# Kernel tuning notes

Measured on AMD Instinct MI355X. Metric: run time of the kernel, lower is better.

The kernel has to match this reference:

```python
import jax, jax.numpy as jnp
import numpy as np

MODEL_DIM = 1024
NUM_HEADS = 16
D_K = MODEL_DIM // NUM_HEADS  # 64
MAX_SEQ_LEN = 3200
B, T = 2, 2048
THETA_BASE = 10000.0


def setup_inputs() -> dict:
    key = jax.random.key(0)
    ks = jax.random.split(key, 5)
    scale = 1.0 / np.sqrt(MODEL_DIM)
    x = jax.random.normal(ks[0], (B, T, MODEL_DIM), dtype=jnp.float32)
    wq = jax.random.normal(ks[1], (MODEL_DIM, MODEL_DIM), dtype=jnp.float32) * scale
    wk = jax.random.normal(ks[2], (MODEL_DIM, MODEL_DIM), dtype=jnp.float32) * scale
    wv = jax.random.normal(ks[3], (MODEL_DIM, MODEL_DIM), dtype=jnp.float32) * scale
    wo = jax.random.normal(ks[4], (MODEL_DIM, MODEL_DIM), dtype=jnp.float32) * scale
    bq = jnp.zeros((MODEL_DIM,), jnp.float32)
    bk = jnp.zeros((MODEL_DIM,), jnp.float32)
    bv = jnp.zeros((MODEL_DIM,), jnp.float32)
    bo = jnp.zeros((MODEL_DIM,), jnp.float32)
    # RoPE tables, exactly as precompute_rotation_matrix: theta duplicated
    # adjacently ([t0,t0,t1,t1,...]).
    theta = THETA_BASE ** (jnp.arange(D_K // 2, dtype=jnp.float32) * (-2.0 / D_K))
    ang = jnp.outer(jnp.arange(MAX_SEQ_LEN, dtype=jnp.float32), theta)  # [L, d/2]
    ang = jnp.repeat(ang, 2, axis=-1)  # [L, d]
    return {
        "x": x, "wq": wq, "bq": bq, "wk": wk, "bk": bk,
        "wv": wv, "bv": bv, "wo": wo, "bo": bo,
        "cos": jnp.cos(ang), "sin": jnp.sin(ang),
    }


def reference(x, wq, bq, wk, bk, wv, bv, wo, bo, cos, sin):
    b, t, dm = x.shape
    h, d = NUM_HEADS, dm // NUM_HEADS

    # NOTE: original uses .view(b, h, t, d) directly on [b, t, h*d] (no
    # transpose) — a nonstandard head split we replicate faithfully.
    xq = (x @ wq.T + bq).reshape(b, h, t, d)
    xk = (x @ wk.T + bk).reshape(b, h, t, d)
    xv = (x @ wv.T + bv).reshape(b, h, t, d)

    def rot_half(q):
        # pairs are adjacent (2i, 2i+1): out[2i] = -q[2i+1], out[2i+1] = q[2i]
        q2 = q.reshape(b, h, t, d // 2, 2)
        return jnp.stack([-q2[..., 1], q2[..., 0]], axis=-1).reshape(b, h, t, d)

    # NOTE: original indexes cos/sin at the single position `seq_len`
    # (rotation_matrix_cos[:, :, xq.shape[2], :]), broadcasting one row over
    # all positions — replicated faithfully.
    c = cos[t]  # [d]
    s = sin[t]  # [d]
    xq = xq * c + rot_half(xq) * s
    xk = xk * c + rot_half(xk) * s

    scores = jnp.einsum("bhqd,bhkd->bhqk", xq, xk) / np.sqrt(d)
    p = jax.nn.softmax(scores, axis=-1)  # mask='none', dropout=0.0
    o = jnp.einsum("bhqk,bhkd->bhqd", p, xv)
    o = o.transpose(0, 2, 1, 3).reshape(b, t, dm)  # 'b h t d -> b t (h d)'
    return o @ wo.T + bo
```

## Files before the change

### kernel.cpp

```cpp
#include <hip/hip_runtime.h>

typedef _Float16 half8 __attribute__((ext_vector_type(8)));
typedef __fp16 pkh2 __attribute__((ext_vector_type(2)));
typedef float floatx4 __attribute__((ext_vector_type(4)));

#define AS1 __attribute__((address_space(1)))
#define AS3 __attribute__((address_space(3)))


__global__ __launch_bounds__(256) void convert_kernel(
    const float* __restrict__ x, const float* __restrict__ wq,
    const float* __restrict__ wk, const float* __restrict__ wv,
    const float* __restrict__ wo,
    _Float16* __restrict__ xb, _Float16* __restrict__ wqkv,
    _Float16* __restrict__ wob)
{
    int i = (blockIdx.x * 256 + threadIdx.x) * 4;
    const float* src; _Float16* dst; int off;
    if (i < 4194304)      { src = x;  dst = xb;            off = i; }
    else if (i < 5242880) { src = wq; dst = wqkv;          off = i - 4194304; }
    else if (i < 6291456) { src = wk; dst = wqkv + 1048576; off = i - 5242880; }
    else if (i < 7340032) { src = wv; dst = wqkv + 2097152; off = i - 6291456; }
    else                  { src = wo; dst = wob;           off = i - 7340032; }
    float4 v = *(const float4*)(src + off);
    union { uint2 u; pkh2 h[2]; } o;
    o.h[0] = __builtin_amdgcn_cvt_pkrtz(v.x, v.y);
    o.h[1] = __builtin_amdgcn_cvt_pkrtz(v.z, v.w);
    *(uint2*)(dst + off) = o.u;
}

template<bool QKV>
__global__ __launch_bounds__(256) void gemm_kernel(
    const _Float16* __restrict__ A, const _Float16* __restrict__ W,
    const float* __restrict__ b0, const float* __restrict__ b1,
    const float* __restrict__ b2,
    const float* __restrict__ cosr, const float* __restrict__ sinr,
    _Float16* __restrict__ O0, _Float16* __restrict__ O1,
    _Float16* __restrict__ O2, float* __restrict__ Of)
{
    __shared__ __align__(16) _Float16 As[128 * 64];
    __shared__ __align__(16) _Float16 Bs[128 * 64];
    const int tid  = threadIdx.x;
    const int lane = tid & 63, w = tid >> 6;
    const int lrow = lane & 15, quad = lane >> 4;
    const int wr = (w & 1) * 64, wc = (w >> 1) * 64;
    const int arow0 = blockIdx.x * 128;
    const int brow0 = blockIdx.y * 128;

    const int r8 = lane >> 3;
    const int gcol = ((lane & 7) ^ r8) * 8;

    floatx4 acc[4][4] = {};

    for (int kk = 0; kk < 1024; kk += 64) {
        __syncthreads();
        for (int u = 0; u < 4; u++) {
            const int row = w * 32 + u * 8;
            __builtin_amdgcn_global_load_lds(
                (const AS1 unsigned*)(const void*)(A + (size_t)(arow0 + row + r8) * 1024 + kk + gcol),
                (AS3 unsigned*)(void*)(As + row * 64), 16, 0, 0);
            __builtin_amdgcn_global_load_lds(
                (const AS1 unsigned*)(const void*)(W + (size_t)(brow0 + row + r8) * 1024 + kk + gcol),
                (AS3 unsigned*)(void*)(Bs + row * 64), 16, 0, 0);
        }
        __syncthreads();
        for (int ks = 0; ks < 2; ks++) {
            const int swz = ((ks * 4 + quad) ^ (lrow & 7)) * 8;
            half8 af[4], bf[4];
            for (int mt = 0; mt < 4; mt++)
                af[mt] = *(const half8*)&As[(wr + mt * 16 + lrow) * 64 + swz];
            for (int nt = 0; nt < 4; nt++)
                bf[nt] = *(const half8*)&Bs[(wc + nt * 16 + lrow) * 64 + swz];
            for (int mt = 0; mt < 4; mt++)
                for (int nt = 0; nt < 4; nt++)
                    acc[mt][nt] = __builtin_amdgcn_mfma_f32_16x16x32_f16(
                        af[mt], bf[nt], acc[mt][nt], 0, 0, 0);
        }
    }

    if (QKV) {
        const int seg = blockIdx.y >> 3;
        const float* bias = seg == 0 ? b0 : (seg == 1 ? b1 : b2);
        _Float16* out = seg == 0 ? O0 : (seg == 1 ? O1 : O2);
        const int nbase = (blockIdx.y & 7) * 128 + wc;
        for (int nt = 0; nt < 4; nt++) {
            const int n = nbase + nt * 16 + lrow;
            const float bv = bias[n];
            const int dj = n & 63;
            const float cv = cosr[dj], sv = sinr[dj];
            const bool odd = (n & 1) != 0;
            for (int mt = 0; mt < 4; mt++)
                for (int r = 0; r < 4; r++) {
                    float v = acc[mt][nt][r] + bv;
                    if (seg < 2) {
                        float p = __shfl_xor(v, 1, 64);
                        v = odd ? (v * cv + p * sv) : (v * cv - p * sv);
                    }
                    if (seg == 0) v *= 0.125f;
                    int row = arow0 + wr + mt * 16 + quad * 4 + r;
                    out[row * 1024 + n] = (_Float16)v;
                }
        }
    } else {
        const int nbase = blockIdx.y * 128 + wc;
        for (int nt = 0; nt < 4; nt++) {
            const int n = nbase + nt * 16 + lrow;
            const float bv = b0[n];
            for (int mt = 0; mt < 4; mt++)
                for (int r = 0; r < 4; r++) {
                    int row = arow0 + wr + mt * 16 + quad * 4 + r;
                    Of[row * 1024 + n] = acc[mt][nt][r] + bv;
                }
        }
    }
}

__global__ __launch_bounds__(256) void vtrans_kernel(
    const _Float16* __restrict__ V, _Float16* __restrict__ VT)
{
    __shared__ __align__(16) _Float16 T[64][72];
    const int tid = threadIdx.x;
    const int kt = blockIdx.x;
    const int bh = blockIdx.y;
    const int bi = bh >> 4, hi = bh & 15;
    const _Float16* Vh = V + (size_t)(bi * 2048 + hi * 128) * 1024 + kt * 4096;
    const int srow = tid >> 3, sblk = tid & 7;
    union { uint4 u; _Float16 h[8]; } a, b;
    a.u = *(const uint4*)(Vh + (2 * srow) * 64 + sblk * 8);
    b.u = *(const uint4*)(Vh + (2 * srow + 1) * 64 + sblk * 8);
    for (int j = 0; j < 8; j++) {
        union { unsigned u; _Float16 h[2]; } pk;
        pk.h[0] = a.h[j]; pk.h[1] = b.h[j];
        *(unsigned*)&T[sblk * 8 + j][2 * srow] = pk.u;
    }
    __syncthreads();
    const int d = tid >> 2, c = tid & 3;
    _Float16* out = VT + ((size_t)bh * 64 + d) * 2048 + kt * 64 + c * 16;
    *(uint4*)(out)     = *(const uint4*)&T[d][c * 16];
    *(uint4*)(out + 8) = *(const uint4*)&T[d][c * 16 + 8];
}

__global__ __launch_bounds__(256, 3) void attn_kernel(
    const _Float16* __restrict__ Q, const _Float16* __restrict__ K,
    const _Float16* __restrict__ VT, _Float16* __restrict__ O)
{
    __shared__ __align__(16) _Float16 Ks[2][64][72];
    __shared__ __align__(16) _Float16 Vts[2][64][72];
    __shared__ __align__(16) _Float16 Pt[4][32][40];

    const int tid  = threadIdx.x;
    const int lane = tid & 63, w = tid >> 6;
    const int lrow = lane & 15, quad = lane >> 4;
    const int qt = blockIdx.x, bh = blockIdx.y;
    const int bi = bh >> 4, hi = bh & 15;
    const size_t base = (size_t)(bi * 2048 + hi * 128) * 1024;
    const _Float16* Qh  = Q + base;
    const _Float16* Kh  = K + base;
    const _Float16* VTh = VT + (size_t)bh * 131072;

    half8 qf[2][2];
    for (int nt = 0; nt < 2; nt++)
        for (int ks = 0; ks < 2; ks++)
            qf[nt][ks] = *(const half8*)(Qh + (qt * 128 + w * 32 + nt * 16 + lrow) * 64
                                          + ks * 32 + quad * 8);

    floatx4 oacc[4][2] = {};
    float lsum0 = 0.0f, lsum1 = 0.0f;

    const int srow = tid >> 3, sblk = tid & 7;
    const int vd = tid >> 2, vc = tid & 3;

    {
        *(uint4*)&Ks[0][srow][sblk * 8]      = *(const uint4*)(Kh + srow * 64 + sblk * 8);
        *(uint4*)&Ks[0][srow + 32][sblk * 8] = *(const uint4*)(Kh + (srow + 32) * 64 + sblk * 8);
        const _Float16* vsrc = VTh + (size_t)vd * 2048 + vc * 16;
        *(uint4*)&Vts[0][vd][vc * 16]     = *(const uint4*)(vsrc);
        *(uint4*)&Vts[0][vd][vc * 16 + 8] = *(const uint4*)(vsrc + 8);
    }
    __syncthreads();

    const float LOG2E = 1.44269504f;
    const float OFF   = -8.65617025f;

    for (int kt = 0; kt < 32; kt++) {
        const int cur = kt & 1;
        uint4 k0, k1, v0, v1;
        if (kt < 31) {
            const _Float16* Kt = Kh + (kt + 1) * 4096;
            const _Float16* Vt = VTh + (size_t)vd * 2048 + (kt + 1) * 64 + vc * 16;
            k0 = *(const uint4*)(Kt + srow * 64 + sblk * 8);
            k1 = *(const uint4*)(Kt + (srow + 32) * 64 + sblk * 8);
            v0 = *(const uint4*)(Vt);
            v1 = *(const uint4*)(Vt + 8);
        }
        for (int h = 0; h < 2; h++) {
            for (int k2 = 0; k2 < 2; k2++) {
                const int kt4 = h * 2 + k2;
                floatx4 s0 = {}, s1 = {};
                for (int ks = 0; ks < 2; ks++) {
                    half8 af = *(const half8*)&Ks[cur][kt4 * 16 + lrow][ks * 32 + quad * 8];
                    s0 = __builtin_amdgcn_mfma_f32_16x16x32_f16(af, qf[0][ks], s0, 0, 0, 0);
                    s1 = __builtin_amdgcn_mfma_f32_16x16x32_f16(af, qf[1][ks], s1, 0, 0, 0);
                }
                float p00 = __builtin_amdgcn_exp2f(fmaf(s0[0], LOG2E, OFF));
                float p01 = __builtin_amdgcn_exp2f(fmaf(s0[1], LOG2E, OFF));
                float p02 = __builtin_amdgcn_exp2f(fmaf(s0[2], LOG2E, OFF));
                float p03 = __builtin_amdgcn_exp2f(fmaf(s0[3], LOG2E, OFF));
                float p10 = __builtin_amdgcn_exp2f(fmaf(s1[0], LOG2E, OFF));
                float p11 = __builtin_amdgcn_exp2f(fmaf(s1[1], LOG2E, OFF));
                float p12 = __builtin_amdgcn_exp2f(fmaf(s1[2], LOG2E, OFF));
                float p13 = __builtin_amdgcn_exp2f(fmaf(s1[3], LOG2E, OFF));
                lsum0 += p00 + p01 + p02 + p03;
                lsum1 += p10 + p11 + p12 + p13;
                union { uint2 u; pkh2 h2[2]; } pk0, pk1;
                pk0.h2[0] = __builtin_amdgcn_cvt_pkrtz(p00, p01);
                pk0.h2[1] = __builtin_amdgcn_cvt_pkrtz(p02, p03);
                pk1.h2[0] = __builtin_amdgcn_cvt_pkrtz(p10, p11);
                pk1.h2[1] = __builtin_amdgcn_cvt_pkrtz(p12, p13);
                *(uint2*)&Pt[w][lrow][k2 * 16 + quad * 4]      = pk0.u;
                *(uint2*)&Pt[w][16 + lrow][k2 * 16 + quad * 4] = pk1.u;
            }
            half8 bf0 = *(const half8*)&Pt[w][lrow][quad * 8];
            half8 bf1 = *(const half8*)&Pt[w][16 + lrow][quad * 8];
            for (int dt = 0; dt < 4; dt++) {
                half8 av = *(const half8*)&Vts[cur][dt * 16 + lrow][h * 32 + quad * 8];
                oacc[dt][0] = __builtin_amdgcn_mfma_f32_16x16x32_f16(av, bf0, oacc[dt][0], 0, 0, 0);
                oacc[dt][1] = __builtin_amdgcn_mfma_f32_16x16x32_f16(av, bf1, oacc[dt][1], 0, 0, 0);
            }
        }
        if (kt < 31) {
            const int nxt = cur ^ 1;
            *(uint4*)&Ks[nxt][srow][sblk * 8]      = k0;
            *(uint4*)&Ks[nxt][srow + 32][sblk * 8] = k1;
            *(uint4*)&Vts[nxt][vd][vc * 16]     = v0;
            *(uint4*)&Vts[nxt][vd][vc * 16 + 8] = v1;
        }
        __syncthreads();
    }

    lsum0 += __shfl_xor(lsum0, 16, 64); lsum0 += __shfl_xor(lsum0, 32, 64);
    lsum1 += __shfl_xor(lsum1, 16, 64); lsum1 += __shfl_xor(lsum1, 32, 64);
    const float inv0 = 1.0f / lsum0, inv1 = 1.0f / lsum1;
    _Float16* Es = (_Float16*)Ks + w * 2304;
    for (int dt = 0; dt < 4; dt++) {
        union { uint2 u; pkh2 h2[2]; } a0, a1;
        a0.h2[0] = __builtin_amdgcn_cvt_pkrtz(oacc[dt][0][0] * inv0, oacc[dt][0][1] * inv0);
        a0.h2[1] = __builtin_amdgcn_cvt_pkrtz(oacc[dt][0][2] * inv0, oacc[dt][0][3] * inv0);
        a1.h2[0] = __builtin_amdgcn_cvt_pkrtz(oacc[dt][1][0] * inv1, oacc[dt][1][1] * inv1);
        a1.h2[1] = __builtin_amdgcn_cvt_pkrtz(oacc[dt][1][2] * inv1, oacc[dt][1][3] * inv1);
        *(uint2*)&Es[lrow * 72 + dt * 16 + quad * 4]        = a0.u;
        *(uint2*)&Es[(16 + lrow) * 72 + dt * 16 + quad * 4] = a1.u;
    }
    const int rw = lane >> 1, hf = lane & 1;
    const size_t orow = (size_t)(bi * 2048 + qt * 128 + w * 32 + rw) * 1024
                        + hi * 64 + hf * 32;
    for (int i = 0; i < 4; i++)
        *(uint4*)(O + orow + i * 8) = *(const uint4*)&Es[rw * 72 + hf * 32 + i * 8];
}

extern "C" void kernel_launch(void* const* d_in, const int* in_sizes, int n_in,
                              void* d_out, int out_size, void* d_ws, size_t ws_size,
                              hipStream_t stream) {
    const float* x    = (const float*)d_in[0];
    const float* wq   = (const float*)d_in[1];
    const float* bq   = (const float*)d_in[2];
    const float* wk   = (const float*)d_in[3];
    const float* bk   = (const float*)d_in[4];
    const float* wv   = (const float*)d_in[5];
    const float* bv   = (const float*)d_in[6];
    const float* wo   = (const float*)d_in[7];
    const float* bo   = (const float*)d_in[8];
    const float* cosT = (const float*)d_in[9];
    const float* sinT = (const float*)d_in[10];

    _Float16* ws   = (_Float16*)d_ws;
    _Float16* xb   = ws;
    _Float16* wqkv = xb + 4194304;
    _Float16* wob  = wqkv + 3145728;
    _Float16* Qb   = wob + 1048576;
    _Float16* Kb   = Qb + 4194304;
    _Float16* Vb   = Kb + 4194304;
    _Float16* Ob   = Vb + 4194304;
    _Float16* VTb  = xb;

    convert_kernel<<<8192, 256, 0, stream>>>(x, wq, wk, wv, wo, xb, wqkv, wob);
    gemm_kernel<true><<<dim3(32, 24), 256, 0, stream>>>(
        xb, wqkv, bq, bk, bv, cosT + 2048 * 64, sinT + 2048 * 64,
        Qb, Kb, Vb, nullptr);
    vtrans_kernel<<<dim3(32, 32), 256, 0, stream>>>(Vb, VTb);
    attn_kernel<<<dim3(16, 32), 256, 0, stream>>>(Qb, Kb, VTb, Ob);
    gemm_kernel<false><<<dim3(32, 8), 256, 0, stream>>>(
        Ob, wob, bo, nullptr, nullptr, nullptr, nullptr,
        nullptr, nullptr, nullptr, (float*)d_out);
}
```

Measured before the change: 217.7 us.

## Feed softmax probabilities directly from registers into 16x16x16 MFMA for PV

Removes the per-wave LDS staging buffer for P. The exp'd scores' accumulator layout already matches the B operand of the 16x16x16 f16 MFMA, so they are packed in registers and fed straight into the PV product, with V read from LDS in 4-element chunks. This drops the P LDS writes and reads and frees shared memory, and occupancy hint is raised from 3 to 4 blocks per CU. The cost is twice as many smaller MFMAs (16x16x16 instead of 16x16x32) for the PV product and more register pressure under the tighter launch bound.

```diff
diff --git a/kernel.cpp b/kernel.cpp
--- a/kernel.cpp
+++ b/kernel.cpp
@@ -2,6 +2,7 @@
 
 typedef _Float16 half8 __attribute__((ext_vector_type(8)));
 typedef __fp16 pkh2 __attribute__((ext_vector_type(2)));
+typedef __fp16 fp16x4 __attribute__((ext_vector_type(4)));
 typedef float floatx4 __attribute__((ext_vector_type(4)));
 
 #define AS1 __attribute__((address_space(1)))
@@ -140,13 +141,12 @@
     *(uint4*)(out + 8) = *(const uint4*)&T[d][c * 16 + 8];
 }
 
-__global__ __launch_bounds__(256, 3) void attn_kernel(
+__global__ __launch_bounds__(256, 4) void attn_kernel(
     const _Float16* __restrict__ Q, const _Float16* __restrict__ K,
     const _Float16* __restrict__ VT, _Float16* __restrict__ O)
 {
     __shared__ __align__(16) _Float16 Ks[2][64][72];
     __shared__ __align__(16) _Float16 Vts[2][64][72];
-    __shared__ __align__(16) _Float16 Pt[4][32][40];
 
     const int tid  = threadIdx.x;
     const int lane = tid & 63, w = tid >> 6;
@@ -193,39 +193,33 @@
             v0 = *(const uint4*)(Vt);
             v1 = *(const uint4*)(Vt + 8);
         }
-        for (int h = 0; h < 2; h++) {
-            for (int k2 = 0; k2 < 2; k2++) {
-                const int kt4 = h * 2 + k2;
-                floatx4 s0 = {}, s1 = {};
-                for (int ks = 0; ks < 2; ks++) {
-                    half8 af = *(const half8*)&Ks[cur][kt4 * 16 + lrow][ks * 32 + quad * 8];
-                    s0 = __builtin_amdgcn_mfma_f32_16x16x32_f16(af, qf[0][ks], s0, 0, 0, 0);
-                    s1 = __builtin_amdgcn_mfma_f32_16x16x32_f16(af, qf[1][ks], s1, 0, 0, 0);
-                }
-                float p00 = __builtin_amdgcn_exp2f(fmaf(s0[0], LOG2E, OFF));
-                float p01 = __builtin_amdgcn_exp2f(fmaf(s0[1], LOG2E, OFF));
-                float p02 = __builtin_amdgcn_exp2f(fmaf(s0[2], LOG2E, OFF));
-                float p03 = __builtin_amdgcn_exp2f(fmaf(s0[3], LOG2E, OFF));
-                float p10 = __builtin_amdgcn_exp2f(fmaf(s1[0], LOG2E, OFF));
-                float p11 = __builtin_amdgcn_exp2f(fmaf(s1[1], LOG2E, OFF));
-                float p12 = __builtin_amdgcn_exp2f(fmaf(s1[2], LOG2E, OFF));
-                float p13 = __builtin_amdgcn_exp2f(fmaf(s1[3], LOG2E, OFF));
-                lsum0 += p00 + p01 + p02 + p03;
-                lsum1 += p10 + p11 + p12 + p13;
-                union { uint2 u; pkh2 h2[2]; } pk0, pk1;
-                pk0.h2[0] = __builtin_amdgcn_cvt_pkrtz(p00, p01);
-                pk0.h2[1] = __builtin_amdgcn_cvt_pkrtz(p02, p03);
-                pk1.h2[0] = __builtin_amdgcn_cvt_pkrtz(p10, p11);
-                pk1.h2[1] = __builtin_amdgcn_cvt_pkrtz(p12, p13);
-                *(uint2*)&Pt[w][lrow][k2 * 16 + quad * 4]      = pk0.u;
-                *(uint2*)&Pt[w][16 + lrow][k2 * 16 + quad * 4] = pk1.u;
+        for (int kt4 = 0; kt4 < 4; kt4++) {
+            floatx4 s0 = {}, s1 = {};
+            for (int ks = 0; ks < 2; ks++) {
+                half8 af = *(const half8*)&Ks[cur][kt4 * 16 + lrow][ks * 32 + quad * 8];
+                s0 = __builtin_amdgcn_mfma_f32_16x16x32_f16(af, qf[0][ks], s0, 0, 0, 0);
+                s1 = __builtin_amdgcn_mfma_f32_16x16x32_f16(af, qf[1][ks], s1, 0, 0, 0);
             }
-            half8 bf0 = *(const half8*)&Pt[w][lrow][quad * 8];
-            half8 bf1 = *(const half8*)&Pt[w][16 + lrow][quad * 8];
+            float p00 = __builtin_amdgcn_exp2f(fmaf(s0[0], LOG2E, OFF));
+            float p01 = __builtin_amdgcn_exp2f(fmaf(s0[1], LOG2E, OFF));
+            float p02 = __builtin_amdgcn_exp2f(fmaf(s0[2], LOG2E, OFF));
+            float p03 = __builtin_amdgcn_exp2f(fmaf(s0[3], LOG2E, OFF));
+            float p10 = __builtin_amdgcn_exp2f(fmaf(s1[0], LOG2E, OFF));
+            float p11 = __builtin_amdgcn_exp2f(fmaf(s1[1], LOG2E, OFF));
+            float p12 = __builtin_amdgcn_exp2f(fmaf(s1[2], LOG2E, OFF));
+            float p13 = __builtin_amdgcn_exp2f(fmaf(s1[3], LOG2E, OFF));
+            lsum0 += (p00 + p01) + (p02 + p03);
+            lsum1 += (p10 + p11) + (p12 + p13);
+            union { pkh2 h2[2]; fp16x4 f4; } b0u, b1u;
+            b0u.h2[0] = __builtin_amdgcn_cvt_pkrtz(p00, p01);
+            b0u.h2[1] = __builtin_amdgcn_cvt_pkrtz(p02, p03);
+            b1u.h2[0] = __builtin_amdgcn_cvt_pkrtz(p10, p11);
+            b1u.h2[1] = __builtin_amdgcn_cvt_pkrtz(p12, p13);
             for (int dt = 0; dt < 4; dt++) {
-                half8 av = *(const half8*)&Vts[cur][dt * 16 + lrow][h * 32 + quad * 8];
-                oacc[dt][0] = __builtin_amdgcn_mfma_f32_16x16x32_f16(av, bf0, oacc[dt][0], 0, 0, 0);
-                oacc[dt][1] = __builtin_amdgcn_mfma_f32_16x16x32_f16(av, bf1, oacc[dt][1], 0, 0, 0);
+                union { uint2 u; fp16x4 f4; } av;
+                av.u = *(const uint2*)&Vts[cur][dt * 16 + lrow][kt4 * 16 + quad * 4];
+                oacc[dt][0] = __builtin_amdgcn_mfma_f32_16x16x16f16(av.f4, b0u.f4, oacc[dt][0], 0, 0, 0);
+                oacc[dt][1] = __builtin_amdgcn_mfma_f32_16x16x16f16(av.f4, b1u.f4, oacc[dt][1], 0, 0, 0);
             }
         }
         if (kt < 31) {
```

After: 236.4 us. 1.09x slower.

## Give each attention wave 64 query rows with 128-thread blocks

Applied to the files above, without the earlier changes.

The attention kernel now runs two waves per block instead of four, and each wave handles 64 query rows (four 16-row tiles) instead of 32. Each K and V fragment read from LDS then feeds four MFMAs rather than two, which cuts LDS traffic per MFMA. The K/V staging loops and the output epilogue are widened to match the smaller thread count. The cost is more accumulator and Q-fragment registers per thread and only half as many resident waves, so there is less latency hiding on the GPU.

```diff
diff --git a/kernel.cpp b/kernel.cpp
--- a/kernel.cpp
+++ b/kernel.cpp
@@ -140,13 +140,13 @@
     *(uint4*)(out + 8) = *(const uint4*)&T[d][c * 16 + 8];
 }
 
-__global__ __launch_bounds__(256, 3) void attn_kernel(
+__global__ __launch_bounds__(128) void attn_kernel(
     const _Float16* __restrict__ Q, const _Float16* __restrict__ K,
     const _Float16* __restrict__ VT, _Float16* __restrict__ O)
 {
     __shared__ __align__(16) _Float16 Ks[2][64][72];
     __shared__ __align__(16) _Float16 Vts[2][64][72];
-    __shared__ __align__(16) _Float16 Pt[4][32][40];
+    __shared__ __align__(16) _Float16 Pt[2][64][40];
 
     const int tid  = threadIdx.x;
     const int lane = tid & 63, w = tid >> 6;
@@ -158,24 +158,25 @@
     const _Float16* Kh  = K + base;
     const _Float16* VTh = VT + (size_t)bh * 131072;
 
-    half8 qf[2][2];
-    for (int nt = 0; nt < 2; nt++)
+    half8 qf[4][2];
+    for (int nt = 0; nt < 4; nt++)
         for (int ks = 0; ks < 2; ks++)
-            qf[nt][ks] = *(const half8*)(Qh + (qt * 128 + w * 32 + nt * 16 + lrow) * 64
+            qf[nt][ks] = *(const half8*)(Qh + (qt * 128 + w * 64 + nt * 16 + lrow) * 64
                                           + ks * 32 + quad * 8);
 
-    floatx4 oacc[4][2] = {};
-    float lsum0 = 0.0f, lsum1 = 0.0f;
+    floatx4 oacc[4][4] = {};
+    float lsum[4] = {0.0f, 0.0f, 0.0f, 0.0f};
 
     const int srow = tid >> 3, sblk = tid & 7;
     const int vd = tid >> 2, vc = tid & 3;
 
-    {
-        *(uint4*)&Ks[0][srow][sblk * 8]      = *(const uint4*)(Kh + srow * 64 + sblk * 8);
-        *(uint4*)&Ks[0][srow + 32][sblk * 8] = *(const uint4*)(Kh + (srow + 32) * 64 + sblk * 8);
-        const _Float16* vsrc = VTh + (size_t)vd * 2048 + vc * 16;
-        *(uint4*)&Vts[0][vd][vc * 16]     = *(const uint4*)(vsrc);
-        *(uint4*)&Vts[0][vd][vc * 16 + 8] = *(const uint4*)(vsrc + 8);
+    for (int r = 0; r < 4; r++)
+        *(uint4*)&Ks[0][srow + r * 16][sblk * 8] =
+            *(const uint4*)(Kh + (srow + r * 16) * 64 + sblk * 8);
+    for (int d2 = 0; d2 < 2; d2++) {
+        const _Float16* vsrc = VTh + (size_t)(vd + d2 * 32) * 2048 + vc * 16;
+        *(uint4*)&Vts[0][vd + d2 * 32][vc * 16]     = *(const uint4*)(vsrc);
+        *(uint4*)&Vts[0][vd + d2 * 32][vc * 16 + 8] = *(const uint4*)(vsrc + 8);
     }
     __syncthreads();
 
@@ -184,78 +185,87 @@
 
     for (int kt = 0; kt < 32; kt++) {
         const int cur = kt & 1;
-        uint4 k0, k1, v0, v1;
+        uint4 kr[4], vr[4];
         if (kt < 31) {
             const _Float16* Kt = Kh + (kt + 1) * 4096;
-            const _Float16* Vt = VTh + (size_t)vd * 2048 + (kt + 1) * 64 + vc * 16;
-            k0 = *(const uint4*)(Kt + srow * 64 + sblk * 8);
-            k1 = *(const uint4*)(Kt + (srow + 32) * 64 + sblk * 8);
-            v0 = *(const uint4*)(Vt);
-            v1 = *(const uint4*)(Vt + 8);
+            for (int r = 0; r < 4; r++)
+                kr[r] = *(const uint4*)(Kt + (srow + r * 16) * 64 + sblk * 8);
+            for (int d2 = 0; d2 < 2; d2++) {
+                const _Float16* Vt = VTh + (size_t)(vd + d2 * 32) * 2048
+                                     + (kt + 1) * 64 + vc * 16;
+                vr[d2 * 2]     = *(const uint4*)(Vt);
+                vr[d2 * 2 + 1] = *(const uint4*)(Vt + 8);
+            }
         }
         for (int h = 0; h < 2; h++) {
             for (int k2 = 0; k2 < 2; k2++) {
                 const int kt4 = h * 2 + k2;
-                floatx4 s0 = {}, s1 = {};
+                floatx4 s[4] = {};
                 for (int ks = 0; ks < 2; ks++) {
                     half8 af = *(const half8*)&Ks[cur][kt4 * 16 + lrow][ks * 32 + quad * 8];
-                    s0 = __builtin_amdgcn_mfma_f32_16x16x32_f16(af, qf[0][ks], s0, 0, 0, 0);
-                    s1 = __builtin_amdgcn_mfma_f32_16x16x32_f16(af, qf[1][ks], s1, 0, 0, 0);
+                    for (int q = 0; q < 4; q++)
+                        s[q] = __builtin_amdgcn_mfma_f32_16x16x32_f16(
+                            af, qf[q][ks], s[q], 0, 0, 0);
                 }
-                float p00 = __builtin_amdgcn_exp2f(fmaf(s0[0], LOG2E, OFF));
-                float p01 = __builtin_amdgcn_exp2f(fmaf(s0[1], LOG2E, OFF));
-                float p02 = __builtin_amdgcn_exp2f(fmaf(s0[2], LOG2E, OFF));
-                float p03 = __builtin_amdgcn_exp2f(fmaf(s0[3], LOG2E, OFF));
-                float p10 = __builtin_amdgcn_exp2f(fmaf(s1[0], LOG2E, OFF));
-                float p11 = __builtin_amdgcn_exp2f(fmaf(s1[1], LOG2E, OFF));
-                float p12 = __builtin_amdgcn_exp2f(fmaf(s1[2], LOG2E, OFF));
-                float p13 = __builtin_amdgcn_exp2f(fmaf(s1[3], LOG2E, OFF));
-                lsum0 += p00 + p01 + p02 + p03;
-                lsum1 += p10 + p11 + p12 + p13;
-                union { uint2 u; pkh2 h2[2]; } pk0, pk1;
-                pk0.h2[0] = __builtin_amdgcn_cvt_pkrtz(p00, p01);
-                pk0.h2[1] = __builtin_amdgcn_cvt_pkrtz(p02, p03);
-                pk1.h2[0] = __builtin_amdgcn_cvt_pkrtz(p10, p11);
-                pk1.h2[1] = __builtin_amdgcn_cvt_pkrtz(p12, p13);
-                *(uint2*)&Pt[w][lrow][k2 * 16 + quad * 4]      = pk0.u;
-                *(uint2*)&Pt[w][16 + lrow][k2 * 16 + quad * 4] = pk1.u;
+                for (int q = 0; q < 4; q++) {
+                    float p0 = __builtin_amdgcn_exp2f(fmaf(s[q][0], LOG2E, OFF));
+                    float p1 = __builtin_amdgcn_exp2f(fmaf(s[q][1], LOG2E, OFF));
+                    float p2 = __builtin_amdgcn_exp2f(fmaf(s[q][2], LOG2E, OFF));
+                    float p3 = __builtin_amdgcn_exp2f(fmaf(s[q][3], LOG2E, OFF));
+                    lsum[q] += (p0 + p1) + (p2 + p3);
+                    union { uint2 u; pkh2 h2[2]; } pk;
+                    pk.h2[0] = __builtin_amdgcn_cvt_pkrtz(p0, p1);
+                    pk.h2[1] = __builtin_amdgcn_cvt_pkrtz(p2, p3);
+                    *(uint2*)&Pt[w][q * 16 + lrow][k2 * 16 + quad * 4] = pk.u;
+                }
             }
-            half8 bf0 = *(const half8*)&Pt[w][lrow][quad * 8];
-            half8 bf1 = *(const half8*)&Pt[w][16 + lrow][quad * 8];
+            half8 bf[4];
+            for (int q = 0; q < 4; q++)
+                bf[q] = *(const half8*)&Pt[w][q * 16 + lrow][quad * 8];
             for (int dt = 0; dt < 4; dt++) {
                 half8 av = *(const half8*)&Vts[cur][dt * 16 + lrow][h * 32 + quad * 8];
-                oacc[dt][0] = __builtin_amdgcn_mfma_f32_16x16x32_f16(av, bf0, oacc[dt][0], 0, 0, 0);
-                oacc[dt][1] = __builtin_amdgcn_mfma_f32_16x16x32_f16(av, bf1, oacc[dt][1], 0, 0, 0);
+                for (int q = 0; q < 4; q++)
+                    oacc[dt][q] = __builtin_amdgcn_mfma_f32_16x16x32_f16(
+                        av, bf[q], oacc[dt][q], 0, 0, 0);
             }
         }
         if (kt < 31) {
             const int nxt = cur ^ 1;
-            *(uint4*)&Ks[nxt][srow][sblk * 8]      = k0;
-            *(uint4*)&Ks[nxt][srow + 32][sblk * 8] = k1;
-            *(uint4*)&Vts[nxt][vd][vc * 16]     = v0;
-            *(uint4*)&Vts[nxt][vd][vc * 16 + 8] = v1;
+            for (int r = 0; r < 4; r++)
+                *(uint4*)&Ks[nxt][srow + r * 16][sblk * 8] = kr[r];
+            for (int d2 = 0; d2 < 2; d2++) {
+                *(uint4*)&Vts[nxt][vd + d2 * 32][vc * 16]     = vr[d2 * 2];
+                *(uint4*)&Vts[nxt][vd + d2 * 32][vc * 16 + 8] = vr[d2 * 2 + 1];
+            }
         }
         __syncthreads();
     }
 
-    lsum0 += __shfl_xor(lsum0, 16, 64); lsum0 += __shfl_xor(lsum0, 32, 64);
-    lsum1 += __shfl_xor(lsum1, 16, 64); lsum1 += __shfl_xor(lsum1, 32, 64);
-    const float inv0 = 1.0f / lsum0, inv1 = 1.0f / lsum1;
-    _Float16* Es = (_Float16*)Ks + w * 2304;
-    for (int dt = 0; dt < 4; dt++) {
-        union { uint2 u; pkh2 h2[2]; } a0, a1;
-        a0.h2[0] = __builtin_amdgcn_cvt_pkrtz(oacc[dt][0][0] * inv0, oacc[dt][0][1] * inv0);
-        a0.h2[1] = __builtin_amdgcn_cvt_pkrtz(oacc[dt][0][2] * inv0, oacc[dt][0][3] * inv0);
-        a1.h2[0] = __builtin_amdgcn_cvt_pkrtz(oacc[dt][1][0] * inv1, oacc[dt][1][1] * inv1);
-        a1.h2[1] = __builtin_amdgcn_cvt_pkrtz(oacc[dt][1][2] * inv1, oacc[dt][1][3] * inv1);
-        *(uint2*)&Es[lrow * 72 + dt * 16 + quad * 4]        = a0.u;
-        *(uint2*)&Es[(16 + lrow) * 72 + dt * 16 + quad * 4] = a1.u;
-    }
+    float inv[4];
+    for (int q = 0; q < 4; q++) {
+        lsum[q] += __shfl_xor(lsum[q], 16, 64);
+        lsum[q] += __shfl_xor(lsum[q], 32, 64);
+        inv[q] = 1.0f / lsum[q];
+    }
+    _Float16* Es = (_Float16*)Ks + w * 4608;
+    for (int dt = 0; dt < 4; dt++)
+        for (int q = 0; q < 4; q++) {
+            union { uint2 u; pkh2 h2[2]; } a0;
+            a0.h2[0] = __builtin_amdgcn_cvt_pkrtz(oacc[dt][q][0] * inv[q],
+                                                  oacc[dt][q][1] * inv[q]);
+            a0.h2[1] = __builtin_amdgcn_cvt_pkrtz(oacc[dt][q][2] * inv[q],
+                                                  oacc[dt][q][3] * inv[q]);
+            *(uint2*)&Es[(q * 16 + lrow) * 72 + dt * 16 + quad * 4] = a0.u;
+        }
+    __syncthreads();
     const int rw = lane >> 1, hf = lane & 1;
-    const size_t orow = (size_t)(bi * 2048 + qt * 128 + w * 32 + rw) * 1024
-                        + hi * 64 + hf * 32;
-    for (int i = 0; i < 4; i++)
-        *(uint4*)(O + orow + i * 8) = *(const uint4*)&Es[rw * 72 + hf * 32 + i * 8];
+    for (int half = 0; half < 2; half++) {
+        const size_t orow = (size_t)(bi * 2048 + qt * 128 + w * 64 + half * 32 + rw) * 1024
+                            + hi * 64 + hf * 32;
+        for (int i = 0; i < 4; i++)
+            *(uint4*)(O + orow + i * 8) =
+                *(const uint4*)&Es[(half * 32 + rw) * 72 + hf * 32 + i * 8];
+    }
 }
 
 extern "C" void kernel_launch(void* const* d_in, const int* in_sizes, int n_in,
@@ -288,7 +298,7 @@
         xb, wqkv, bq, bk, bv, cosT + 2048 * 64, sinT + 2048 * 64,
         Qb, Kb, Vb, nullptr);
     vtrans_kernel<<<dim3(32, 32), 256, 0, stream>>>(Vb, VTb);
-    attn_kernel<<<dim3(16, 32), 256, 0, stream>>>(Qb, Kb, VTb, Ob);
+    attn_kernel<<<dim3(16, 32), 128, 0, stream>>>(Qb, Kb, VTb, Ob);
     gemm_kernel<false><<<dim3(32, 8), 256, 0, stream>>>(
         Ob, wob, bo, nullptr, nullptr, nullptr, nullptr,
         nullptr, nullptr, nullptr, (float*)d_out);
```

Result: slower. 289.4 us (+32.9%).
